# Kernel optimization log

Measured on AMD Instinct MI355X. Metric: run time of the kernel, lower is better.

## Reference

```python
import jax, jax.numpy as jnp
import numpy as np

B, L, C = 8, 4096, 256  # batches, points per batch, channels
C8 = C // 8             # query/key projection dim


def setup_inputs() -> dict:
    key = jax.random.key(0)
    ks = jax.random.split(key, 8)
    feats = jax.random.normal(ks[0], (B * L, C), dtype=jnp.float32)
    s_in = 1.0 / np.sqrt(C)
    Wq = jax.random.normal(ks[1], (C8, C), dtype=jnp.float32) * s_in
    bq = jax.random.normal(ks[2], (C8,), dtype=jnp.float32) * 0.01
    Wk = jax.random.normal(ks[3], (C8, C), dtype=jnp.float32) * s_in
    bk = jax.random.normal(ks[4], (C8,), dtype=jnp.float32) * 0.01
    Wv = jax.random.normal(ks[5], (C, C), dtype=jnp.float32) * s_in
    bv = jax.random.normal(ks[6], (C,), dtype=jnp.float32) * 0.01
    # torch init is gamma=0 which zeroes the attention branch; use a nonzero
    # scalar so the attention path contributes to output/gradients.
    gamma = jnp.float32(0.5)
    return {"feats": feats, "Wq": Wq, "bq": bq, "Wk": Wk, "bk": bk,
            "Wv": Wv, "bv": bv, "gamma": gamma,
            "batch_size": B, "points_per_batch": L}


def reference(feats, Wq, bq, Wk, bk, Wv, bv, gamma, batch_size, points_per_batch):
    n, c = feats.shape
    x = feats.reshape(batch_size, points_per_batch, c)  # [B, L, C]
    # conv1d with kernel_size=1 == per-point linear projection
    q = jnp.einsum('blc,dc->bld', x, Wq) + bq  # [B, L, C8]
    k = jnp.einsum('blc,dc->bld', x, Wk) + bk  # [B, L, C8]
    v = jnp.einsum('blc,dc->bld', x, Wv) + bv  # [B, L, C]
    energy = jnp.einsum('bid,bjd->bij', q, k)  # unscaled scores [B, L, L]
    attn = jax.nn.softmax(energy, axis=-1)
    # torch: out[c, l] = sum_j V[c, j] * attn[l, j]  -> [B, C, L]
    out_cl = jnp.einsum('bjc,blj->bcl', v, attn)
    # faithful to torch .view(batch_size, C): raw reshape of [C, L] -> [L, C]
    out = out_cl.reshape(batch_size, points_per_batch, c)
    y = gamma * out + x
    return y.reshape(n, c)
```

## Files before the change

### kernel.cpp

```cpp
#include <hip/hip_runtime.h>

#define LOG2E 1.44269504088896340736f

typedef __attribute__((ext_vector_type(4))) float  f32x4;
typedef __attribute__((ext_vector_type(8))) __bf16 bf16x8;
typedef __attribute__((ext_vector_type(4))) __bf16 bf16x4;

static __device__ __forceinline__ f32x4 mfma16(bf16x8 a, bf16x8 b, f32x4 c) {
  return __builtin_amdgcn_mfma_f32_16x16x32_bf16(a, b, c, 0, 0, 0);
}


__global__ void cvt_f32_to_bf16(const float* __restrict__ s, __bf16* __restrict__ d, int n4) {
  const int stride = gridDim.x * blockDim.x;
  for (int i = blockIdx.x * blockDim.x + threadIdx.x; i < n4; i += stride) {
    const float4 v = reinterpret_cast<const float4*>(s)[i];
    bf16x4 o = { (__bf16)v.x, (__bf16)v.y, (__bf16)v.z, (__bf16)v.w };
    reinterpret_cast<bf16x4*>(d)[i] = o;
  }
}

__global__ __launch_bounds__(256) void qk_proj(
    const __bf16* __restrict__ x, const __bf16* __restrict__ wq, const __bf16* __restrict__ wk,
    const float* __restrict__ bq, const float* __restrict__ bk,
    __bf16* __restrict__ Qh, __bf16* __restrict__ Ql,
    __bf16* __restrict__ Kp)
{
  const int w = threadIdx.x >> 6, lane = threadIdx.x & 63;
  const int lo = lane & 15, hi = lane >> 4;
  const int m0 = blockIdx.x * 64 + w * 16;
  f32x4 acc[4] = {};
  for (int ks = 0; ks < 8; ++ks) {
    const bf16x8 a = *reinterpret_cast<const bf16x8*>(x + (size_t)(m0 + lo) * 256 + ks * 32 + hi * 8);
    #pragma unroll
    for (int nt = 0; nt < 4; ++nt) {
      const int d = nt * 16 + lo;
      const __bf16* wrow = (nt < 2) ? (wq + d * 256) : (wk + (d - 32) * 256);
      const bf16x8 bfr = *reinterpret_cast<const bf16x8*>(wrow + ks * 32 + hi * 8);
      acc[nt] = mfma16(a, bfr, acc[nt]);
    }
  }
  #pragma unroll
  for (int nt = 0; nt < 4; ++nt) {
    const int d = nt * 16 + lo;
    const float bias = (nt < 2) ? bq[d] : bk[d - 32];
    #pragma unroll
    for (int r = 0; r < 4; ++r) {
      const size_t row = m0 + hi * 4 + r;
      float v = acc[nt][r] + bias;
      if (nt < 2) {
        v *= LOG2E;
        const __bf16 vh = (__bf16)v;
        const __bf16 vl = (__bf16)(v - (float)vh);
        Qh[row * 32 + d] = vh;
        Ql[row * 32 + d] = vl;
      } else {
        const int dd = d - 32;
        const __bf16 vh = (__bf16)v;
        const __bf16 vl = (__bf16)(v - (float)vh);
        const int sH = (dd >> 3) ^ ((int)row & 7);
        const int sL = (4 | (dd >> 3)) ^ ((int)row & 7);
        Kp[row * 64 + sH * 8 + (dd & 7)] = vh;
        Kp[row * 64 + sL * 8 + (dd & 7)] = vl;
      }
    }
  }
}

__global__ __launch_bounds__(256) void v_proj(
    const __bf16* __restrict__ x, const __bf16* __restrict__ wv, const float* __restrict__ bv,
    __bf16* __restrict__ VT)
{
  const int w = threadIdx.x >> 6, lane = threadIdx.x & 63;
  const int lo = lane & 15, hi = lane >> 4;
  const int bn = blockIdx.x & 511, bc = blockIdx.x >> 9;
  const int n0 = bn * 64;
  const int c0 = bc * 64 + w * 16;
  f32x4 acc[4] = {};
  for (int ks = 0; ks < 8; ++ks) {
    const bf16x8 a = *reinterpret_cast<const bf16x8*>(wv + (size_t)(c0 + lo) * 256 + ks * 32 + hi * 8);
    #pragma unroll
    for (int nt = 0; nt < 4; ++nt) {
      const bf16x8 bfr = *reinterpret_cast<const bf16x8*>(x + (size_t)(n0 + nt * 16 + lo) * 256 + ks * 32 + hi * 8);
      acc[nt] = mfma16(a, bfr, acc[nt]);
    }
  }
  const int bb = n0 >> 12;
  #pragma unroll
  for (int nt = 0; nt < 4; ++nt) {
    const int nl = n0 + nt * 16 + lo;
    #pragma unroll
    for (int r = 0; r < 4; ++r) {
      const int c = c0 + hi * 4 + r;
      VT[(size_t)(bb * 256 + c) * 4096 + (nl & 4095)] = (__bf16)(acc[nt][r] + bv[c]);
    }
  }
}

__global__ __launch_bounds__(256, 2) void attn_kernel(
    const __bf16* __restrict__ Qhi, const __bf16* __restrict__ Qlo,
    const __bf16* __restrict__ Kp, const __bf16* __restrict__ VT,
    const float* __restrict__ feats, const float* __restrict__ gptr,
    float* __restrict__ out)
{
  __shared__ alignas(16) __bf16 klds[2][4096];
  __shared__ alignas(16) __bf16 pbuf[2][4096];
  __shared__ float lred[64];

  const int tid  = threadIdx.x;
  const int w    = tid >> 6, lane = tid & 63;
  const int lo   = lane & 15, hi = lane >> 4;
  const int b    = blockIdx.x & 7;
  const int qt   = blockIdx.x >> 3;
  const int qblk = qt * 64;
  const int qw   = qblk + w * 16;
  const int cw   = w * 64;

  const size_t qrow = (size_t)(b * 4096 + qw + lo) * 32 + hi * 8;
  const bf16x8 qh = *reinterpret_cast<const bf16x8*>(Qhi + qrow);
  const bf16x8 ql = *reinterpret_cast<const bf16x8*>(Qlo + qrow);

  const __bf16* kbase = Kp + (size_t)b * 4096 * 64;
  const __bf16* vbase = VT + (size_t)b * 256 * 4096;
  const __bf16* vp[4];
  #pragma unroll
  for (int ct = 0; ct < 4; ++ct)
    vp[ct] = vbase + (size_t)(cw + ct * 16 + lo) * 4096 + hi * 8;

  int koff_h[4], koff_l[4];
  #pragma unroll
  for (int jt = 0; jt < 4; ++jt) {
    const int r = jt * 16 + lo;
    koff_h[jt] = r * 128 + ((hi ^ (lo & 7)) << 4);
    koff_l[jt] = r * 128 + (((4 | hi) ^ (lo & 7)) << 4);
  }

  const int swz = (lo & 7) << 4;
  const int pwr = (w * 16 + lo) * 128;

  f32x4 o[4][4] = {};
  f32x4 lacc4 = {0.f, 0.f, 0.f, 0.f};

  #define STAGE_K(JB, BUF)                                                        \
    {                                                                             \
      const __bf16* g_ = kbase + (size_t)(JB) * 64;                               \
      _Pragma("unroll")                                                           \
      for (int ss = 0; ss < 2; ++ss) {                                            \
        const int seg = w + ss * 4;                                               \
        __builtin_amdgcn_global_load_lds(                                         \
            (const __attribute__((address_space(1))) void*)(g_ + seg * 512 + lane * 8), \
            (__attribute__((address_space(3))) void*)(&klds[BUF][seg * 512]),     \
            16, 0, 0);                                                            \
      }                                                                           \
    }

  STAGE_K(0, 0);
  bf16x8 vcur[8];
  #pragma unroll
  for (int ks = 0; ks < 2; ++ks)
    #pragma unroll
    for (int ct = 0; ct < 4; ++ct)
      vcur[ks * 4 + ct] = *reinterpret_cast<const bf16x8*>(vp[ct] + ks * 32);
  asm volatile("s_waitcnt vmcnt(0)" ::: "memory");
  __builtin_amdgcn_s_barrier();

  #pragma unroll 2
  for (int t = 0; t < 64; ++t) {
    const int jb  = t * 64;
    const int jn  = (jb + 64) & 4095;
    const int cur = t & 1, nxt = cur ^ 1;

    const char* kb = (const char*)klds[cur];
    bf16x8 kh[4], kl[4];
    #pragma unroll
    for (int jt = 0; jt < 4; ++jt) {
      kh[jt] = *reinterpret_cast<const bf16x8*>(kb + koff_h[jt]);
      kl[jt] = *reinterpret_cast<const bf16x8*>(kb + koff_l[jt]);
    }

    STAGE_K(jn, nxt);
    asm volatile("" ::: "memory");
    __builtin_amdgcn_sched_barrier(0);

    bf16x8 vnxt[8];
    #pragma unroll
    for (int ks = 0; ks < 2; ++ks)
      #pragma unroll
      for (int ct = 0; ct < 4; ++ct)
        vnxt[ks * 4 + ct] = *reinterpret_cast<const bf16x8*>(vp[ct] + jn + ks * 32);

    f32x4 s[4];
    #pragma unroll
    for (int jt = 0; jt < 4; ++jt) {
      f32x4 acc = {0.f, 0.f, 0.f, 0.f};
      acc = mfma16(kh[jt], qh, acc);
      acc = mfma16(kl[jt], qh, acc);
      acc = mfma16(kh[jt], ql, acc);
      s[jt] = acc;
    }

    char* const pw = (char*)pbuf[cur] + pwr;
    #pragma unroll
    for (int jt = 0; jt < 4; ++jt) {
      f32x4 p4;
      #pragma unroll
      for (int r = 0; r < 4; ++r) p4[r] = __builtin_amdgcn_exp2f(s[jt][r]);
      lacc4 += p4;
      bf16x4 pk = { (__bf16)p4[0], (__bf16)p4[1], (__bf16)p4[2], (__bf16)p4[3] };
      *reinterpret_cast<bf16x4*>(pw + ((jt * 32 + hi * 8) ^ swz)) = pk;
    }

    asm volatile("s_waitcnt vmcnt(8) lgkmcnt(0)" ::: "memory");
    __builtin_amdgcn_sched_barrier(0);
    __builtin_amdgcn_s_barrier();
    asm volatile("" ::: "memory");
    __builtin_amdgcn_sched_barrier(0);

    const char* const pr = (const char*)pbuf[cur];
    __builtin_amdgcn_s_setprio(1);
    #pragma unroll
    for (int ks = 0; ks < 2; ++ks) {
      bf16x8 pf[4];
      #pragma unroll
      for (int qt2 = 0; qt2 < 4; ++qt2)
        pf[qt2] = *reinterpret_cast<const bf16x8*>(pr + (qt2 * 16 + lo) * 128 + ((ks * 64 + hi * 16) ^ swz));
      #pragma unroll
      for (int qt2 = 0; qt2 < 4; ++qt2)
        #pragma unroll
        for (int ct = 0; ct < 4; ++ct)
          o[qt2][ct] = mfma16(pf[qt2], vcur[ks * 4 + ct], o[qt2][ct]);
    }
    __builtin_amdgcn_s_setprio(0);

    #pragma unroll
    for (int i = 0; i < 8; ++i) vcur[i] = vnxt[i];
  }
  #undef STAGE_K

  float lacc = lacc4[0] + lacc4[1] + lacc4[2] + lacc4[3];
  lacc += __shfl_xor(lacc, 16);
  lacc += __shfl_xor(lacc, 32);
  __syncthreads();
  if (lane < 16) lred[w * 16 + lo] = lacc;
  __syncthreads();

  const float g = gptr[0];
  const size_t obase = (size_t)b * (256 * 4096);
  #pragma unroll
  for (int qt2 = 0; qt2 < 4; ++qt2) {
    float inv[4];
    #pragma unroll
    for (int r = 0; r < 4; ++r) inv[r] = g / lred[qt2 * 16 + hi * 4 + r];
    const int q_lo = qblk + qt2 * 16 + hi * 4;
    #pragma unroll
    for (int ct = 0; ct < 4; ++ct) {
      const int c = cw + ct * 16 + lo;
      const size_t idx = obase + (size_t)c * 4096 + q_lo;
      const float4 xr = *reinterpret_cast<const float4*>(feats + idx);
      float4 y;
      y.x = o[qt2][ct][0] * inv[0] + xr.x;
      y.y = o[qt2][ct][1] * inv[1] + xr.y;
      y.z = o[qt2][ct][2] * inv[2] + xr.z;
      y.w = o[qt2][ct][3] * inv[3] + xr.w;
      *reinterpret_cast<float4*>(out + idx) = y;
    }
  }
}

extern "C" void kernel_launch(void* const* d_in, const int* in_sizes, int n_in,
                              void* d_out, int out_size, void* d_ws, size_t ws_size,
                              hipStream_t stream) {
  const float* feats = (const float*)d_in[0];
  const float* Wq    = (const float*)d_in[1];
  const float* bq    = (const float*)d_in[2];
  const float* Wk    = (const float*)d_in[3];
  const float* bk    = (const float*)d_in[4];
  const float* Wv    = (const float*)d_in[5];
  const float* bv    = (const float*)d_in[6];
  const float* gamma = (const float*)d_in[7];
  float* out = (float*)d_out;

  char* ws = (char*)d_ws;
  const size_t SZ_X  = 16777216;
  const size_t SZ_Q  = 2097152;
  const size_t SZ_KP = 4194304;
  const size_t SZ_VT = 16777216;
  const size_t NEED = SZ_X + 2 * SZ_Q + SZ_KP + SZ_VT + 2 * 16384 + 131072;
  if (ws_size < NEED) return;

  __bf16* xb  = (__bf16*)(ws);
  __bf16* Qh  = (__bf16*)(ws + SZ_X);
  __bf16* Ql  = (__bf16*)(ws + SZ_X + SZ_Q);
  __bf16* Kpp = (__bf16*)(ws + SZ_X + 2 * SZ_Q);
  __bf16* VT  = (__bf16*)(ws + SZ_X + 2 * SZ_Q + SZ_KP);
  __bf16* wqb = (__bf16*)(ws + SZ_X + 2 * SZ_Q + SZ_KP + SZ_VT);
  __bf16* wkb = wqb + 32 * 256;
  __bf16* wvb = wkb + 32 * 256;

  cvt_f32_to_bf16<<<2048, 256, 0, stream>>>(feats, xb, 8388608 / 4);
  cvt_f32_to_bf16<<<8,    256, 0, stream>>>(Wq, wqb, 8192 / 4);
  cvt_f32_to_bf16<<<8,    256, 0, stream>>>(Wk, wkb, 8192 / 4);
  cvt_f32_to_bf16<<<64,   256, 0, stream>>>(Wv, wvb, 65536 / 4);

  qk_proj<<<512, 256, 0, stream>>>(xb, wqb, wkb, bq, bk, Qh, Ql, Kpp);
  v_proj <<<2048, 256, 0, stream>>>(xb, wvb, bv, VT);
  attn_kernel<<<512, 256, 0, stream>>>(Qh, Ql, Kpp, VT, feats, gamma, out);
}
```

Baseline: 204.7 us.

## Software-pipeline attention loop: overlap QK/softmax of next tile with PV of previous

Restructures the attention main loop so each iteration computes QK scores and softmax for tile t while running the PV MFMAs for tile t-1, with a prologue and an epilogue PV step. This removes the per-iteration serialization between the barrier and the PV matmul, letting exp/LDS writes overlap with tensor work. It also fuses the three small weight conversion launches into one kernel to cut launch overhead. The pipelined schedule raises register pressure and complicates the double-buffer indexing of pbuf and V.

```diff
diff --git a/kernel.cpp b/kernel.cpp
--- a/kernel.cpp
+++ b/kernel.cpp
@@ -18,6 +18,19 @@
     bf16x4 o = { (__bf16)v.x, (__bf16)v.y, (__bf16)v.z, (__bf16)v.w };
     reinterpret_cast<bf16x4*>(d)[i] = o;
   }
+}
+
+__global__ __launch_bounds__(256) void cvt_weights(
+    const float* __restrict__ wq, const float* __restrict__ wk, const float* __restrict__ wv,
+    __bf16* __restrict__ dq, __bf16* __restrict__ dk, __bf16* __restrict__ dv) {
+  const int i = blockIdx.x * 256 + threadIdx.x;
+  const float* s; __bf16* d; int off;
+  if (i < 2048)      { s = wq; d = dq; off = i; }
+  else if (i < 4096) { s = wk; d = dk; off = i - 2048; }
+  else               { s = wv; d = dv; off = i - 4096; }
+  const float4 v = reinterpret_cast<const float4*>(s)[off];
+  bf16x4 o = { (__bf16)v.x, (__bf16)v.y, (__bf16)v.z, (__bf16)v.w };
+  reinterpret_cast<bf16x4*>(d)[off] = o;
 }
 
 __global__ __launch_bounds__(256) void qk_proj(
@@ -140,6 +153,7 @@
 
   f32x4 o[4][4] = {};
   f32x4 lacc4 = {0.f, 0.f, 0.f, 0.f};
+  bf16x8 vcur[8];
 
   #define STAGE_K(JB, BUF)                                                        \
     {                                                                             \
@@ -154,29 +168,90 @@
       }                                                                           \
     }
 
+  #define QK_STEP(KBUF, SDST)                                                     \
+    {                                                                             \
+      const char* kb_ = (const char*)(KBUF);                                      \
+      _Pragma("unroll")                                                           \
+      for (int jt = 0; jt < 4; ++jt) {                                            \
+        const bf16x8 kh_ = *reinterpret_cast<const bf16x8*>(kb_ + koff_h[jt]);    \
+        const bf16x8 kl_ = *reinterpret_cast<const bf16x8*>(kb_ + koff_l[jt]);    \
+        f32x4 a_ = {0.f, 0.f, 0.f, 0.f};                                          \
+        a_ = mfma16(kh_, qh, a_);                                                 \
+        a_ = mfma16(kl_, qh, a_);                                                 \
+        a_ = mfma16(kh_, ql, a_);                                                 \
+        SDST[jt] = a_;                                                            \
+      }                                                                           \
+    }
+
+  #define SOFTMAX_STEP(SSRC, PWBUF)                                               \
+    {                                                                             \
+      char* const pw_ = (char*)(PWBUF) + pwr;                                     \
+      _Pragma("unroll")                                                           \
+      for (int jt = 0; jt < 4; ++jt) {                                            \
+        f32x4 p4;                                                                 \
+        _Pragma("unroll")                                                         \
+        for (int r = 0; r < 4; ++r) p4[r] = __builtin_amdgcn_exp2f(SSRC[jt][r]);  \
+        lacc4 += p4;                                                              \
+        bf16x4 pk = { (__bf16)p4[0], (__bf16)p4[1], (__bf16)p4[2], (__bf16)p4[3] }; \
+        *reinterpret_cast<bf16x4*>(pw_ + ((jt * 32 + hi * 8) ^ swz)) = pk;        \
+      }                                                                           \
+    }
+
+  #define PV_STEP(PRBUF, VARR)                                                    \
+    {                                                                             \
+      const char* const pr_ = (const char*)(PRBUF);                               \
+      __builtin_amdgcn_s_setprio(1);                                              \
+      _Pragma("unroll")                                                           \
+      for (int ks = 0; ks < 2; ++ks) {                                            \
+        bf16x8 pf[4];                                                             \
+        _Pragma("unroll")                                                         \
+        for (int q2 = 0; q2 < 4; ++q2)                                            \
+          pf[q2] = *reinterpret_cast<const bf16x8*>(pr_ + (q2 * 16 + lo) * 128 + ((ks * 64 + hi * 16) ^ swz)); \
+        _Pragma("unroll")                                                         \
+        for (int q2 = 0; q2 < 4; ++q2)                                            \
+          _Pragma("unroll")                                                       \
+          for (int ct = 0; ct < 4; ++ct)                                          \
+            o[q2][ct] = mfma16(pf[q2], VARR[ks * 4 + ct], o[q2][ct]);             \
+      }                                                                           \
+      __builtin_amdgcn_s_setprio(0);                                              \
+    }
+
+  #define BARRIER_SEQ()                                                           \
+    asm volatile("s_waitcnt vmcnt(8) lgkmcnt(0)" ::: "memory");                   \
+    __builtin_amdgcn_sched_barrier(0);                                            \
+    __builtin_amdgcn_s_barrier();                                                 \
+    asm volatile("" ::: "memory");                                                \
+    __builtin_amdgcn_sched_barrier(0);
+
   STAGE_K(0, 0);
-  bf16x8 vcur[8];
-  #pragma unroll
-  for (int ks = 0; ks < 2; ++ks)
-    #pragma unroll
-    for (int ct = 0; ct < 4; ++ct)
-      vcur[ks * 4 + ct] = *reinterpret_cast<const bf16x8*>(vp[ct] + ks * 32);
   asm volatile("s_waitcnt vmcnt(0)" ::: "memory");
   __builtin_amdgcn_s_barrier();
 
+  {
+    f32x4 s[4];
+    QK_STEP(klds[0], s);
+    SOFTMAX_STEP(s, pbuf[0]);
+    STAGE_K(64, 1);
+    asm volatile("" ::: "memory");
+    __builtin_amdgcn_sched_barrier(0);
+    #pragma unroll
+    for (int ks = 0; ks < 2; ++ks)
+      #pragma unroll
+      for (int ct = 0; ct < 4; ++ct)
+        vcur[ks * 4 + ct] = *reinterpret_cast<const bf16x8*>(vp[ct] + ks * 32);
+    BARRIER_SEQ();
+  }
+
   #pragma unroll 2
-  for (int t = 0; t < 64; ++t) {
+  for (int t = 1; t < 64; ++t) {
+    const int cur = t & 1, nxt = cur ^ 1;
     const int jb  = t * 64;
     const int jn  = (jb + 64) & 4095;
-    const int cur = t & 1, nxt = cur ^ 1;
-
-    const char* kb = (const char*)klds[cur];
-    bf16x8 kh[4], kl[4];
-    #pragma unroll
-    for (int jt = 0; jt < 4; ++jt) {
-      kh[jt] = *reinterpret_cast<const bf16x8*>(kb + koff_h[jt]);
-      kl[jt] = *reinterpret_cast<const bf16x8*>(kb + koff_l[jt]);
-    }
+
+    f32x4 s[4];
+    QK_STEP(klds[cur], s);
+    PV_STEP(pbuf[nxt], vcur);
+    SOFTMAX_STEP(s, pbuf[cur]);
 
     STAGE_K(jn, nxt);
     asm volatile("" ::: "memory");
@@ -187,55 +262,21 @@
     for (int ks = 0; ks < 2; ++ks)
       #pragma unroll
       for (int ct = 0; ct < 4; ++ct)
-        vnxt[ks * 4 + ct] = *reinterpret_cast<const bf16x8*>(vp[ct] + jn + ks * 32);
-
-    f32x4 s[4];
-    #pragma unroll
-    for (int jt = 0; jt < 4; ++jt) {
-      f32x4 acc = {0.f, 0.f, 0.f, 0.f};
-      acc = mfma16(kh[jt], qh, acc);
-      acc = mfma16(kl[jt], qh, acc);
-      acc = mfma16(kh[jt], ql, acc);
-      s[jt] = acc;
-    }
-
-    char* const pw = (char*)pbuf[cur] + pwr;
-    #pragma unroll
-    for (int jt = 0; jt < 4; ++jt) {
-      f32x4 p4;
-      #pragma unroll
-      for (int r = 0; r < 4; ++r) p4[r] = __builtin_amdgcn_exp2f(s[jt][r]);
-      lacc4 += p4;
-      bf16x4 pk = { (__bf16)p4[0], (__bf16)p4[1], (__bf16)p4[2], (__bf16)p4[3] };
-      *reinterpret_cast<bf16x4*>(pw + ((jt * 32 + hi * 8) ^ swz)) = pk;
-    }
-
-    asm volatile("s_waitcnt vmcnt(8) lgkmcnt(0)" ::: "memory");
-    __builtin_amdgcn_sched_barrier(0);
-    __builtin_amdgcn_s_barrier();
-    asm volatile("" ::: "memory");
-    __builtin_amdgcn_sched_barrier(0);
-
-    const char* const pr = (const char*)pbuf[cur];
-    __builtin_amdgcn_s_setprio(1);
-    #pragma unroll
-    for (int ks = 0; ks < 2; ++ks) {
-      bf16x8 pf[4];
-      #pragma unroll
-      for (int qt2 = 0; qt2 < 4; ++qt2)
-        pf[qt2] = *reinterpret_cast<const bf16x8*>(pr + (qt2 * 16 + lo) * 128 + ((ks * 64 + hi * 16) ^ swz));
-      #pragma unroll
-      for (int qt2 = 0; qt2 < 4; ++qt2)
-        #pragma unroll
-        for (int ct = 0; ct < 4; ++ct)
-          o[qt2][ct] = mfma16(pf[qt2], vcur[ks * 4 + ct], o[qt2][ct]);
-    }
-    __builtin_amdgcn_s_setprio(0);
+        vnxt[ks * 4 + ct] = *reinterpret_cast<const bf16x8*>(vp[ct] + jb + ks * 32);
+
+    BARRIER_SEQ();
 
     #pragma unroll
     for (int i = 0; i < 8; ++i) vcur[i] = vnxt[i];
   }
+
+  PV_STEP(pbuf[1], vcur);
+
   #undef STAGE_K
+  #undef QK_STEP
+  #undef SOFTMAX_STEP
+  #undef PV_STEP
+  #undef BARRIER_SEQ
 
   float lacc = lacc4[0] + lacc4[1] + lacc4[2] + lacc4[3];
   lacc += __shfl_xor(lacc, 16);
@@ -298,9 +339,7 @@
   __bf16* wvb = wkb + 32 * 256;
 
   cvt_f32_to_bf16<<<2048, 256, 0, stream>>>(feats, xb, 8388608 / 4);
-  cvt_f32_to_bf16<<<8,    256, 0, stream>>>(Wq, wqb, 8192 / 4);
-  cvt_f32_to_bf16<<<8,    256, 0, stream>>>(Wk, wkb, 8192 / 4);
-  cvt_f32_to_bf16<<<64,   256, 0, stream>>>(Wv, wvb, 65536 / 4);
+  cvt_weights<<<80, 256, 0, stream>>>(Wq, Wk, Wv, wqb, wkb, wvb);
 
   qk_proj<<<512, 256, 0, stream>>>(xb, wqb, wkb, bq, bk, Qh, Ql, Kpp);
   v_proj <<<2048, 256, 0, stream>>>(xb, wvb, bv, VT);
```

Result: faster. 197.3 us (-3.6%).
